# Kernel tuning notes

Measured on AMD Instinct MI355X. Metric: run time of the kernel, lower is better.

Reference implementation:

```python
import jax, jax.numpy as jnp
import numpy as np

N_HEADS, D_MODEL, D_HEAD = 16, 1024, 64
INIT_RANGE = 0.02
BATCH, SEQ = 4, 2048


def setup_inputs() -> dict:
    key = jax.random.key(0)
    k0, k1, k2, k3, k4 = jax.random.split(key, 5)
    resid = jax.random.normal(k0, (BATCH, SEQ, D_MODEL), dtype=jnp.float32)
    w_q = INIT_RANGE * jax.random.normal(k1, (N_HEADS, D_MODEL, D_HEAD), dtype=jnp.float32)
    w_k = INIT_RANGE * jax.random.normal(k2, (N_HEADS, D_MODEL, D_HEAD), dtype=jnp.float32)
    w_v = INIT_RANGE * jax.random.normal(k3, (N_HEADS, D_MODEL, D_HEAD), dtype=jnp.float32)
    w_o = INIT_RANGE * jax.random.normal(k4, (N_HEADS, D_HEAD, D_MODEL), dtype=jnp.float32)
    return {"resid": resid, "w_q": w_q, "w_k": w_k, "w_v": w_v, "w_o": w_o}


def reference(resid, w_q, w_k, w_v, w_o):
    # resid: [b, s, m]; w_q/k/v: [h, m, d]; w_o: [h, d, m]
    qs = jnp.einsum('bsm,hmd->bhsd', resid, w_q)
    ks = jnp.einsum('bsm,hmd->bhsd', resid, w_k)
    vs = jnp.einsum('bsm,hmd->bhsd', resid, w_v)
    attn = jnp.einsum('bhqd,bhkd->bhqk', qs, ks)  # full O(n^2) scores
    s = attn.shape[-1]
    causal = jnp.tril(jnp.ones((s, s), dtype=bool))  # True = keep
    attn = jnp.where(causal, attn, -jnp.inf)
    attn = jax.nn.softmax(attn / jnp.sqrt(jnp.float32(D_HEAD)), axis=-1)
    z = jnp.einsum('bhqk,bhkd->bhqd', attn, vs)
    out = jnp.einsum('bhsd,hdm->bsm', z, w_o)
    return out
```

## Files before the change

kernel.cpp:

```cpp
#include <hip/hip_runtime.h>


typedef __attribute__((ext_vector_type(8))) short short8;
typedef __attribute__((ext_vector_type(4))) float f32x4;
typedef __attribute__((ext_vector_type(16))) float f32x16;

#define GLDS16(g, l) __builtin_amdgcn_global_load_lds(                        \
    (const __attribute__((address_space(1))) unsigned int*)(g),               \
    (__attribute__((address_space(3))) unsigned int*)(l), 16, 0, 0)

static __device__ __forceinline__ unsigned short f2b(float f) {
  union { float f; unsigned u; } c; c.f = f;
  unsigned r = c.u + 0x7fffu + ((c.u >> 16) & 1u);
  return (unsigned short)(r >> 16);
}

static __device__ __forceinline__ int swzc(int row, int c) {
  return (c & ~31) | ((((c >> 3) & 3) ^ ((row >> 1) & 3)) << 3) | (c & 7);
}

__global__ void k_cast(const float* __restrict__ x, unsigned short* __restrict__ o, int n4) {
  int i = blockIdx.x * blockDim.x + threadIdx.x;
  if (i >= n4) return;
  float4 v = reinterpret_cast<const float4*>(x)[i];
  ushort4 u;
  u.x = f2b(v.x); u.y = f2b(v.y); u.z = f2b(v.z); u.w = f2b(v.w);
  const int flat = i * 4;
  const int row = flat >> 10, c = flat & 1023;
  *reinterpret_cast<ushort4*>(&o[row * 1024 + swzc(row, c)]) = u;
}

__global__ void k_trans_qkv(const float* __restrict__ wq, const float* __restrict__ wk,
                            const float* __restrict__ wv, unsigned short* __restrict__ o) {
  __shared__ float t[64][65];
  int blk = blockIdx.x;
  int mt = blk & 15;
  int h = (blk >> 4) & 15;
  int which = blk >> 8;
  const float* w = which == 0 ? wq : (which == 1 ? wk : wv);
  int tid = threadIdx.x;
  int m0 = mt * 64;
  #pragma unroll
  for (int rep = 0; rep < 16; ++rep) {
    int idx = rep * 256 + tid;
    int r = idx >> 6, c = idx & 63;
    t[r][c] = w[(h * 1024 + m0 + r) * 64 + c];
  }
  __syncthreads();
  #pragma unroll
  for (int rep = 0; rep < 16; ++rep) {
    int idx = rep * 256 + tid;
    int dr = idx >> 6, mc = idx & 63;
    const int row = which * 1024 + h * 64 + dr;
    o[row * 1024 + swzc(dr, m0 + mc)] = f2b(t[mc][dr]);
  }
}

__global__ void k_trans_wo(const float* __restrict__ wo, unsigned short* __restrict__ o) {
  __shared__ float t[64][65];
  int blk = blockIdx.x;
  int mt = blk & 15, kt = blk >> 4;
  int tid = threadIdx.x;
  int k0 = kt * 64, m0 = mt * 64;
  #pragma unroll
  for (int rep = 0; rep < 16; ++rep) {
    int idx = rep * 256 + tid;
    int r = idx >> 6, c = idx & 63;
    t[r][c] = wo[(k0 + r) * 1024 + m0 + c];
  }
  __syncthreads();
  #pragma unroll
  for (int rep = 0; rep < 16; ++rep) {
    int idx = rep * 256 + tid;
    int r = idx >> 6, c = idx & 63;
    o[(m0 + r) * 1024 + swzc(r, k0 + c)] = f2b(t[c][r]);
  }
}

__global__ __launch_bounds__(256) void k_gemm_qkv(const unsigned short* __restrict__ A,
                                                  const unsigned short* __restrict__ Bt,
                                                  unsigned short* __restrict__ Qb,
                                                  unsigned short* __restrict__ Kc,
                                                  unsigned short* __restrict__ Vc) {
  __shared__ unsigned short As[2][128 * 32];
  __shared__ unsigned short Bs[2][128 * 32];
  const int bm = blockIdx.x, bn = blockIdx.y;
  const int tid = threadIdx.x;
  const int lane = tid & 63, wid = tid >> 6;
  const int wr = wid >> 1, wc = wid & 1;
  const int fr = lane & 15, fq = lane >> 4;

  f32x4 acc[4][4];
  #pragma unroll
  for (int i = 0; i < 4; ++i)
    #pragma unroll
    for (int n = 0; n < 4; ++n) acc[i][n] = f32x4{0.f, 0.f, 0.f, 0.f};

  const int arow = tid >> 2, acol = (tid & 3) * 8;
  const int lds0 = tid * 8, lds1 = (tid + 256) * 8;
  const unsigned short* aG0 = A + (bm * 128 + arow) * 1024 + acol;
  const unsigned short* aG1 = A + (bm * 128 + arow + 64) * 1024 + acol;
  const unsigned short* bG0 = Bt + (bn * 128 + arow) * 1024 + acol;
  const unsigned short* bG1 = Bt + (bn * 128 + arow + 64) * 1024 + acol;

  const int rowA = (wr * 64 + fr) * 32;
  const int rowB = (wc * 64 + fr) * 32;
  const int slot = ((fq ^ ((fr >> 1) & 3)) << 3);

  for (int k0 = 0; k0 < 1024; k0 += 64) {
    __syncthreads();
    GLDS16(aG0 + k0,      As[0] + lds0);
    GLDS16(aG1 + k0,      As[0] + lds1);
    GLDS16(aG0 + k0 + 32, As[1] + lds0);
    GLDS16(aG1 + k0 + 32, As[1] + lds1);
    GLDS16(bG0 + k0,      Bs[0] + lds0);
    GLDS16(bG1 + k0,      Bs[0] + lds1);
    GLDS16(bG0 + k0 + 32, Bs[1] + lds0);
    GLDS16(bG1 + k0 + 32, Bs[1] + lds1);
    asm volatile("s_waitcnt vmcnt(0)" ::: "memory");
    __syncthreads();
    #pragma unroll
    for (int p = 0; p < 2; ++p) {
      short8 a[4], b[4];
      #pragma unroll
      for (int i = 0; i < 4; ++i)
        a[i] = *reinterpret_cast<const short8*>(As[p] + rowA + i * 512 + slot);
      #pragma unroll
      for (int n = 0; n < 4; ++n)
        b[n] = *reinterpret_cast<const short8*>(Bs[p] + rowB + n * 512 + slot);
      #pragma unroll
      for (int i = 0; i < 4; ++i)
        #pragma unroll
        for (int n = 0; n < 4; ++n)
          acc[i][n] = __builtin_amdgcn_mfma_f32_16x16x32_bf16(a[i], b[n], acc[i][n], 0, 0, 0);
    }
  }

  const float CS = 0.125f * 1.44269504088896340736f;
  const int colb = bn * 128 + wc * 64 + fr;
  const int rowb = bm * 128 + wr * 64 + fq * 4;
  #pragma unroll
  for (int n = 0; n < 4; ++n) {
    const int col = colb + n * 16;
    const int which = col >> 10, rc = col & 1023;
    const int h = rc >> 6, d = rc & 63;
    #pragma unroll
    for (int i = 0; i < 4; ++i) {
      const int row = rowb + i * 16;
      const int b_ = row >> 11, s = row & 2047;
      const int bh = b_ * 16 + h;
      if (which == 2) {
        const int c = s >> 5, kk = s & 31;
        const int r = d >> 1;
        const int sl = (((d & 1) * 4 + (kk >> 3)) ^ (r & 7));
        ushort4 v;
        v.x = f2b(acc[i][n][0]); v.y = f2b(acc[i][n][1]);
        v.z = f2b(acc[i][n][2]); v.w = f2b(acc[i][n][3]);
        *reinterpret_cast<ushort4*>(
            &Vc[((size_t)(bh * 64 + c)) * 2048 + r * 64 + sl * 8 + (kk & 7)]) = v;
      } else if (which == 1) {
        #pragma unroll
        for (int j = 0; j < 4; ++j) {
          const int ss = s + j;
          const int c = ss >> 5, r = ss & 31;
          const int dsw = (((d >> 3) ^ (r & 7)) << 3) | (d & 7);
          Kc[(((size_t)(bh * 64 + c)) * 32 + r) * 64 + dsw] = f2b(acc[i][n][j]);
        }
      } else {
        unsigned short* dst = Qb + ((size_t)bh * 2048 + s) * 64 + d;
        #pragma unroll
        for (int j = 0; j < 4; ++j) dst[j * 64] = f2b(acc[i][n][j] * CS);
      }
    }
  }
}


static __device__ __forceinline__ f32x16 mfma32(short8 a, short8 b, f32x16 c) {
  return __builtin_amdgcn_mfma_f32_32x32x16_bf16(a, b, c, 0, 0, 0);
}

template<bool MASKED>
static __device__ __forceinline__ void compute_chunk(
    const unsigned short* __restrict__ Kl, const unsigned short* __restrict__ Vl,
    int q, int hi,
    const short8& Qf0, const short8& Qf1, const short8& Qf2, const short8& Qf3,
    f32x16& accA, f32x16& accB, float& lsum) {
  const int qs = q & 7;
  const short8 kf0 = *reinterpret_cast<const short8*>(Kl + q * 64 + (((0 + hi) ^ qs) << 3));
  const short8 kf1 = *reinterpret_cast<const short8*>(Kl + q * 64 + (((2 + hi) ^ qs) << 3));
  const short8 kf2 = *reinterpret_cast<const short8*>(Kl + q * 64 + (((4 + hi) ^ qs) << 3));
  const short8 kf3 = *reinterpret_cast<const short8*>(Kl + q * 64 + (((6 + hi) ^ qs) << 3));
  const int vr = q >> 1, vs = (q & 1) * 4, vw = vr & 7;
  const short8 v00 = *reinterpret_cast<const short8*>(Vl + vr * 64 + (((vs + hi) ^ vw) << 3));
  const short8 v01 = *reinterpret_cast<const short8*>(Vl + vr * 64 + (((vs + 2 + hi) ^ vw) << 3));
  const short8 v10 = *reinterpret_cast<const short8*>(Vl + (vr + 16) * 64 + (((vs + hi) ^ vw) << 3));
  const short8 v11 = *reinterpret_cast<const short8*>(Vl + (vr + 16) * 64 + (((vs + 2 + hi) ^ vw) << 3));

  f32x16 s = {0.f,0.f,0.f,0.f,0.f,0.f,0.f,0.f,0.f,0.f,0.f,0.f,0.f,0.f,0.f,0.f};
  s = mfma32(kf0, Qf0, s);
  s = mfma32(kf1, Qf1, s);
  s = mfma32(kf2, Qf2, s);
  s = mfma32(kf3, Qf3, s);

  float p[16];
  #pragma unroll
  for (int r = 0; r < 16; ++r) {
    if (MASKED) {
      const int kr = (r & 3) + 8 * (r >> 2) + 4 * hi;
      p[r] = (kr <= q) ? __builtin_amdgcn_exp2f(s[r]) : 0.f;
    } else {
      p[r] = __builtin_amdgcn_exp2f(s[r]);
    }
  }
  float t0 = (p[0] + p[1]) + (p[2] + p[3]);
  float t1 = (p[4] + p[5]) + (p[6] + p[7]);
  float t2 = (p[8] + p[9]) + (p[10] + p[11]);
  float t3 = (p[12] + p[13]) + (p[14] + p[15]);
  lsum += (t0 + t1) + (t2 + t3);

  unsigned W[8], X[8];
  #pragma unroll
  for (int i = 0; i < 8; ++i)
    asm("v_cvt_pk_bf16_f32 %0, %1, %2" : "=v"(W[i]) : "v"(p[2 * i]), "v"(p[2 * i + 1]));
  #pragma unroll
  for (int i = 0; i < 8; ++i) X[i] = __shfl_xor(W[i], 32);

  union { unsigned u[4]; short8 v; } fa0, fa1;
  fa0.u[0] = hi ? X[2] : W[0];
  fa0.u[1] = hi ? X[3] : W[1];
  fa0.u[2] = hi ? W[2] : X[0];
  fa0.u[3] = hi ? W[3] : X[1];
  fa1.u[0] = hi ? X[6] : W[4];
  fa1.u[1] = hi ? X[7] : W[5];
  fa1.u[2] = hi ? W[6] : X[4];
  fa1.u[3] = hi ? W[7] : X[5];

  accA = mfma32(fa0.v, v00, accA);
  accA = mfma32(fa1.v, v01, accA);
  accB = mfma32(fa0.v, v10, accB);
  accB = mfma32(fa1.v, v11, accB);
}

static __device__ __forceinline__ void store_tile(unsigned short* __restrict__ Zb,
    int b_, int h, int q0, int q, int hi,
    const f32x16& a0, const f32x16& a1, float lsum) {
  const float lt = lsum + __shfl_xor(lsum, 32);
  const float rl = 1.f / lt;
  #pragma unroll
  for (int r = 0; r < 16; ++r) {
    const int qr = (r & 3) + 8 * (r >> 2) + 4 * hi;
    const float rlr = __shfl(rl, qr);
    const int row = b_ * 2048 + q0 + qr;
    const int sl = (((q >> 3) ^ ((qr >> 1) & 3)) << 3) + (q & 7);
    unsigned short* dst = Zb + (size_t)row * 1024 + h * 64;
    dst[sl]      = f2b(a0[r] * rlr);
    dst[32 + sl] = f2b(a1[r] * rlr);
  }
}

__global__ __launch_bounds__(256, 2) void k_attn(const unsigned short* __restrict__ Qb,
                                                 const unsigned short* __restrict__ Kc,
                                                 const unsigned short* __restrict__ Vc,
                                                 unsigned short* __restrict__ Zb) {
  __shared__ __align__(16) unsigned short Kbuf[2][2048];
  __shared__ __align__(16) unsigned short Vbuf[2][2048];
  const int tid = threadIdx.x;
  const int lane = tid & 63, w = tid >> 6;
  const int q = lane & 31, hi = lane >> 5;
  const int bid = blockIdx.x;
  const int bh = (bid & 7) * 8 + ((bid >> 3) & 7);
  const int P1 = bid >> 6;
  const int b_ = bh >> 4, h = bh & 15;

  const unsigned short* Qbh = Qb + (size_t)bh * 2048 * 64;
  const unsigned short* Kch = Kc + (size_t)bh * 64 * 2048;
  const unsigned short* Vch = Vc + (size_t)bh * 64 * 2048;

  #pragma unroll 1
  for (int t = 0; t < 2; ++t) {
    const int P = t ? (15 - P1) : P1;
    const int q0 = 128 * P + 32 * w;
    const int cmax = 4 * P + w;
    const int C = 4 * P + 4;

    const unsigned short* Qp = Qbh + (size_t)(q0 + q) * 64 + hi * 8;
    const short8 Qf0 = *reinterpret_cast<const short8*>(Qp);
    const short8 Qf1 = *reinterpret_cast<const short8*>(Qp + 16);
    const short8 Qf2 = *reinterpret_cast<const short8*>(Qp + 32);
    const short8 Qf3 = *reinterpret_cast<const short8*>(Qp + 48);

    f32x16 a0 = {0.f,0.f,0.f,0.f,0.f,0.f,0.f,0.f,0.f,0.f,0.f,0.f,0.f,0.f,0.f,0.f};
    f32x16 a1 = a0;
    float l = 0.f;

    GLDS16(Kch + tid * 8, &Kbuf[0][tid * 8]);
    GLDS16(Vch + tid * 8, &Vbuf[0][tid * 8]);

    for (int c = 0; c < C; ++c) {
      if (c + 1 < C) {
        const int par = (c + 1) & 1;
        GLDS16(Kch + (size_t)(c + 1) * 2048 + tid * 8, &Kbuf[par][tid * 8]);
        GLDS16(Vch + (size_t)(c + 1) * 2048 + tid * 8, &Vbuf[par][tid * 8]);
        asm volatile("s_waitcnt vmcnt(2)" ::: "memory");
      } else {
        asm volatile("s_waitcnt vmcnt(0)" ::: "memory");
      }
      __syncthreads();
      if (c <= cmax) {
        const int par = c & 1;
        if (c == cmax)
          compute_chunk<true>(Kbuf[par], Vbuf[par], q, hi, Qf0, Qf1, Qf2, Qf3, a0, a1, l);
        else
          compute_chunk<false>(Kbuf[par], Vbuf[par], q, hi, Qf0, Qf1, Qf2, Qf3, a0, a1, l);
      }
      __syncthreads();
    }
    store_tile(Zb, b_, h, q0, q, hi, a0, a1, l);
  }
}

__global__ __launch_bounds__(256) void k_gemm_out(const unsigned short* __restrict__ A,
                                                  const unsigned short* __restrict__ Bt,
                                                  float* __restrict__ Out) {
  __shared__ unsigned short As[2][128 * 32];
  __shared__ unsigned short Bs[2][128 * 32];
  const int bm = blockIdx.x, bn = blockIdx.y;
  const int tid = threadIdx.x;
  const int lane = tid & 63, wid = tid >> 6;
  const int wr = wid >> 1, wc = wid & 1;
  const int fr = lane & 15, fq = lane >> 4;

  f32x4 acc[4][4];
  #pragma unroll
  for (int i = 0; i < 4; ++i)
    #pragma unroll
    for (int n = 0; n < 4; ++n) acc[i][n] = f32x4{0.f, 0.f, 0.f, 0.f};

  const int arow = tid >> 2, acol = (tid & 3) * 8;
  const int lds0 = tid * 8, lds1 = (tid + 256) * 8;
  const unsigned short* aG0 = A + (bm * 128 + arow) * 1024 + acol;
  const unsigned short* aG1 = A + (bm * 128 + arow + 64) * 1024 + acol;
  const unsigned short* bG0 = Bt + (bn * 128 + arow) * 1024 + acol;
  const unsigned short* bG1 = Bt + (bn * 128 + arow + 64) * 1024 + acol;

  const int rowA = (wr * 64 + fr) * 32;
  const int rowB = (wc * 64 + fr) * 32;
  const int slot = ((fq ^ ((fr >> 1) & 3)) << 3);

  for (int k0 = 0; k0 < 1024; k0 += 64) {
    __syncthreads();
    GLDS16(aG0 + k0,      As[0] + lds0);
    GLDS16(aG1 + k0,      As[0] + lds1);
    GLDS16(aG0 + k0 + 32, As[1] + lds0);
    GLDS16(aG1 + k0 + 32, As[1] + lds1);
    GLDS16(bG0 + k0,      Bs[0] + lds0);
    GLDS16(bG1 + k0,      Bs[0] + lds1);
    GLDS16(bG0 + k0 + 32, Bs[1] + lds0);
    GLDS16(bG1 + k0 + 32, Bs[1] + lds1);
    asm volatile("s_waitcnt vmcnt(0)" ::: "memory");
    __syncthreads();
    #pragma unroll
    for (int p = 0; p < 2; ++p) {
      short8 a[4], b[4];
      #pragma unroll
      for (int i = 0; i < 4; ++i)
        a[i] = *reinterpret_cast<const short8*>(As[p] + rowA + i * 512 + slot);
      #pragma unroll
      for (int n = 0; n < 4; ++n)
        b[n] = *reinterpret_cast<const short8*>(Bs[p] + rowB + n * 512 + slot);
      #pragma unroll
      for (int i = 0; i < 4; ++i)
        #pragma unroll
        for (int n = 0; n < 4; ++n)
          acc[i][n] = __builtin_amdgcn_mfma_f32_16x16x32_bf16(a[i], b[n], acc[i][n], 0, 0, 0);
    }
  }

  const int colb = bn * 128 + wc * 64 + fr;
  const int rowb = bm * 128 + wr * 64 + fq * 4;
  #pragma unroll
  for (int n = 0; n < 4; ++n) {
    const int col = colb + n * 16;
    #pragma unroll
    for (int i = 0; i < 4; ++i) {
      const int row = rowb + i * 16;
      #pragma unroll
      for (int j = 0; j < 4; ++j) Out[(size_t)(row + j) * 1024 + col] = acc[i][n][j];
    }
  }
}

extern "C" void kernel_launch(void* const* d_in, const int* in_sizes, int n_in,
                              void* d_out, int out_size, void* d_ws, size_t ws_size,
                              hipStream_t stream) {
  const float* resid = (const float*)d_in[0];
  const float* w_q = (const float*)d_in[1];
  const float* w_k = (const float*)d_in[2];
  const float* w_v = (const float*)d_in[3];
  const float* w_o = (const float*)d_in[4];
  float* out = (float*)d_out;

  char* ws = (char*)d_ws;
  const size_t MB = 1u << 20;
  unsigned short* Xb = (unsigned short*)(ws);
  unsigned short* W3 = (unsigned short*)(ws + 16 * MB);
  unsigned short* Wo = (unsigned short*)(ws + 22 * MB);
  unsigned short* Qb = (unsigned short*)(ws + 24 * MB);
  unsigned short* Kc = (unsigned short*)(ws + 40 * MB);
  unsigned short* Vc = (unsigned short*)(ws + 56 * MB);
  unsigned short* Zb = Xb;

  hipLaunchKernelGGL(k_cast, dim3(8192), dim3(256), 0, stream, resid, Xb, 8192 * 1024 / 4);
  hipLaunchKernelGGL(k_trans_qkv, dim3(768), dim3(256), 0, stream, w_q, w_k, w_v, W3);
  hipLaunchKernelGGL(k_trans_wo, dim3(256), dim3(256), 0, stream, w_o, Wo);
  hipLaunchKernelGGL(k_gemm_qkv, dim3(64, 24), dim3(256), 0, stream, Xb, W3, Qb, Kc, Vc);
  hipLaunchKernelGGL(k_attn, dim3(512), dim3(256), 0, stream, Qb, Kc, Vc, Zb);
  hipLaunchKernelGGL(k_gemm_out, dim3(64, 8), dim3(256), 0, stream, Zb, Wo, out);
}
```

Measured before the change: 168.6 us.

## Double-buffer GEMM K-loop loads and triple-buffer attention K/V chunks

Both GEMM kernels now keep two LDS stage sets, issuing the next 64-wide K slice's global-to-LDS loads before computing on the current one, so memory latency overlaps with MFMA work instead of being waited on serially. The attention kernel moves from double to triple buffering of K/V chunks with a prefetch distance of two, which also drops one barrier per iteration. The cost is more LDS (64KB per GEMM block, 24KB per attention block), which may reduce occupancy.

```diff
diff --git a/kernel.cpp b/kernel.cpp
--- a/kernel.cpp
+++ b/kernel.cpp
@@ -77,13 +77,42 @@
   }
 }
 
+#define QKV_STAGE(k0, SET)                                                    \
+    GLDS16(aG0 + (k0),      As[SET] + lds0);                                  \
+    GLDS16(aG1 + (k0),      As[SET] + lds1);                                  \
+    GLDS16(aG0 + (k0) + 32, As[SET] + 4096 + lds0);                           \
+    GLDS16(aG1 + (k0) + 32, As[SET] + 4096 + lds1);                           \
+    GLDS16(bG0 + (k0),      Bs[SET] + lds0);                                  \
+    GLDS16(bG1 + (k0),      Bs[SET] + lds1);                                  \
+    GLDS16(bG0 + (k0) + 32, Bs[SET] + 4096 + lds0);                           \
+    GLDS16(bG1 + (k0) + 32, Bs[SET] + 4096 + lds1);
+
+#define GEMM_COMPUTE(SET)                                                     \
+    _Pragma("unroll")                                                         \
+    for (int p = 0; p < 2; ++p) {                                             \
+      short8 a[4], b[4];                                                      \
+      _Pragma("unroll")                                                       \
+      for (int i = 0; i < 4; ++i)                                             \
+        a[i] = *reinterpret_cast<const short8*>(As[SET] + p * 4096 + rowA + i * 512 + slot); \
+      _Pragma("unroll")                                                       \
+      for (int n = 0; n < 4; ++n)                                             \
+        b[n] = *reinterpret_cast<const short8*>(Bs[SET] + p * 4096 + rowB + n * 512 + slot); \
+      _Pragma("unroll")                                                       \
+      for (int i = 0; i < 4; ++i)                                             \
+        _Pragma("unroll")                                                     \
+        for (int n = 0; n < 4; ++n)                                           \
+          acc[i][n] = __builtin_amdgcn_mfma_f32_16x16x32_bf16(a[i], b[n], acc[i][n], 0, 0, 0); \
+    }
+
+#define VM0 asm volatile("s_waitcnt vmcnt(0)" ::: "memory")
+
 __global__ __launch_bounds__(256) void k_gemm_qkv(const unsigned short* __restrict__ A,
                                                   const unsigned short* __restrict__ Bt,
                                                   unsigned short* __restrict__ Qb,
                                                   unsigned short* __restrict__ Kc,
                                                   unsigned short* __restrict__ Vc) {
-  __shared__ unsigned short As[2][128 * 32];
-  __shared__ unsigned short Bs[2][128 * 32];
+  __shared__ unsigned short As[2][8192];
+  __shared__ unsigned short Bs[2][8192];
   const int bm = blockIdx.x, bn = blockIdx.y;
   const int tid = threadIdx.x;
   const int lane = tid & 63, wid = tid >> 6;
@@ -107,33 +136,16 @@
   const int rowB = (wc * 64 + fr) * 32;
   const int slot = ((fq ^ ((fr >> 1) & 3)) << 3);
 
-  for (int k0 = 0; k0 < 1024; k0 += 64) {
+  QKV_STAGE(0, 0);
+  for (int s2 = 0; s2 < 16; s2 += 2) {
+    VM0;
     __syncthreads();
-    GLDS16(aG0 + k0,      As[0] + lds0);
-    GLDS16(aG1 + k0,      As[0] + lds1);
-    GLDS16(aG0 + k0 + 32, As[1] + lds0);
-    GLDS16(aG1 + k0 + 32, As[1] + lds1);
-    GLDS16(bG0 + k0,      Bs[0] + lds0);
-    GLDS16(bG1 + k0,      Bs[0] + lds1);
-    GLDS16(bG0 + k0 + 32, Bs[1] + lds0);
-    GLDS16(bG1 + k0 + 32, Bs[1] + lds1);
-    asm volatile("s_waitcnt vmcnt(0)" ::: "memory");
+    QKV_STAGE((s2 + 1) * 64, 1);
+    GEMM_COMPUTE(0);
+    VM0;
     __syncthreads();
-    #pragma unroll
-    for (int p = 0; p < 2; ++p) {
-      short8 a[4], b[4];
-      #pragma unroll
-      for (int i = 0; i < 4; ++i)
-        a[i] = *reinterpret_cast<const short8*>(As[p] + rowA + i * 512 + slot);
-      #pragma unroll
-      for (int n = 0; n < 4; ++n)
-        b[n] = *reinterpret_cast<const short8*>(Bs[p] + rowB + n * 512 + slot);
-      #pragma unroll
-      for (int i = 0; i < 4; ++i)
-        #pragma unroll
-        for (int n = 0; n < 4; ++n)
-          acc[i][n] = __builtin_amdgcn_mfma_f32_16x16x32_bf16(a[i], b[n], acc[i][n], 0, 0, 0);
-    }
+    if (s2 + 2 < 16) { QKV_STAGE((s2 + 2) * 64, 0); }
+    GEMM_COMPUTE(1);
   }
 
   const float CS = 0.125f * 1.44269504088896340736f;
@@ -263,8 +275,8 @@
                                                  const unsigned short* __restrict__ Kc,
                                                  const unsigned short* __restrict__ Vc,
                                                  unsigned short* __restrict__ Zb) {
-  __shared__ __align__(16) unsigned short Kbuf[2][2048];
-  __shared__ __align__(16) unsigned short Vbuf[2][2048];
+  __shared__ __align__(16) unsigned short Kbuf[3][2048];
+  __shared__ __align__(16) unsigned short Vbuf[3][2048];
   const int tid = threadIdx.x;
   const int lane = tid & 63, w = tid >> 6;
   const int q = lane & 31, hi = lane >> 5;
@@ -294,27 +306,29 @@
     f32x16 a1 = a0;
     float l = 0.f;
 
-    GLDS16(Kch + tid * 8, &Kbuf[0][tid * 8]);
-    GLDS16(Vch + tid * 8, &Vbuf[0][tid * 8]);
-
+    __syncthreads();
+    GLDS16(Kch + tid * 8,        &Kbuf[0][tid * 8]);
+    GLDS16(Vch + tid * 8,        &Vbuf[0][tid * 8]);
+    GLDS16(Kch + 2048 + tid * 8, &Kbuf[1][tid * 8]);
+    GLDS16(Vch + 2048 + tid * 8, &Vbuf[1][tid * 8]);
+
+    int ci = 0, si = 2;
     for (int c = 0; c < C; ++c) {
-      if (c + 1 < C) {
-        const int par = (c + 1) & 1;
-        GLDS16(Kch + (size_t)(c + 1) * 2048 + tid * 8, &Kbuf[par][tid * 8]);
-        GLDS16(Vch + (size_t)(c + 1) * 2048 + tid * 8, &Vbuf[par][tid * 8]);
-        asm volatile("s_waitcnt vmcnt(2)" ::: "memory");
-      } else {
-        asm volatile("s_waitcnt vmcnt(0)" ::: "memory");
+      if (c == C - 1) { asm volatile("s_waitcnt vmcnt(0)" ::: "memory"); }
+      else            { asm volatile("s_waitcnt vmcnt(2)" ::: "memory"); }
+      __syncthreads();
+      if (c + 2 < C) {
+        GLDS16(Kch + (size_t)(c + 2) * 2048 + tid * 8, &Kbuf[si][tid * 8]);
+        GLDS16(Vch + (size_t)(c + 2) * 2048 + tid * 8, &Vbuf[si][tid * 8]);
       }
-      __syncthreads();
       if (c <= cmax) {
-        const int par = c & 1;
         if (c == cmax)
-          compute_chunk<true>(Kbuf[par], Vbuf[par], q, hi, Qf0, Qf1, Qf2, Qf3, a0, a1, l);
+          compute_chunk<true>(Kbuf[ci], Vbuf[ci], q, hi, Qf0, Qf1, Qf2, Qf3, a0, a1, l);
         else
-          compute_chunk<false>(Kbuf[par], Vbuf[par], q, hi, Qf0, Qf1, Qf2, Qf3, a0, a1, l);
+          compute_chunk<false>(Kbuf[ci], Vbuf[ci], q, hi, Qf0, Qf1, Qf2, Qf3, a0, a1, l);
       }
-      __syncthreads();
+      ci = (ci + 1 == 3) ? 0 : ci + 1;
+      si = (si + 1 == 3) ? 0 : si + 1;
     }
     store_tile(Zb, b_, h, q0, q, hi, a0, a1, l);
   }
@@ -323,8 +337,8 @@
 __global__ __launch_bounds__(256) void k_gemm_out(const unsigned short* __restrict__ A,
                                                   const unsigned short* __restrict__ Bt,
                                                   float* __restrict__ Out) {
-  __shared__ unsigned short As[2][128 * 32];
-  __shared__ unsigned short Bs[2][128 * 32];
+  __shared__ unsigned short As[2][8192];
+  __shared__ unsigned short Bs[2][8192];
   const int bm = blockIdx.x, bn = blockIdx.y;
   const int tid = threadIdx.x;
   const int lane = tid & 63, wid = tid >> 6;
@@ -348,33 +362,16 @@
   const int rowB = (wc * 64 + fr) * 32;
   const int slot = ((fq ^ ((fr >> 1) & 3)) << 3);
 
-  for (int k0 = 0; k0 < 1024; k0 += 64) {
+  QKV_STAGE(0, 0);
+  for (int s2 = 0; s2 < 16; s2 += 2) {
+    VM0;
     __syncthreads();
-    GLDS16(aG0 + k0,      As[0] + lds0);
-    GLDS16(aG1 + k0,      As[0] + lds1);
-    GLDS16(aG0 + k0 + 32, As[1] + lds0);
-    GLDS16(aG1 + k0 + 32, As[1] + lds1);
-    GLDS16(bG0 + k0,      Bs[0] + lds0);
-    GLDS16(bG1 + k0,      Bs[0] + lds1);
-    GLDS16(bG0 + k0 + 32, Bs[1] + lds0);
-    GLDS16(bG1 + k0 + 32, Bs[1] + lds1);
-    asm volatile("s_waitcnt vmcnt(0)" ::: "memory");
+    QKV_STAGE((s2 + 1) * 64, 1);
+    GEMM_COMPUTE(0);
+    VM0;
     __syncthreads();
-    #pragma unroll
-    for (int p = 0; p < 2; ++p) {
-      short8 a[4], b[4];
-      #pragma unroll
-      for (int i = 0; i < 4; ++i)
-        a[i] = *reinterpret_cast<const short8*>(As[p] + rowA + i * 512 + slot);
-      #pragma unroll
-      for (int n = 0; n < 4; ++n)
-        b[n] = *reinterpret_cast<const short8*>(Bs[p] + rowB + n * 512 + slot);
-      #pragma unroll
-      for (int i = 0; i < 4; ++i)
-        #pragma unroll
-        for (int n = 0; n < 4; ++n)
-          acc[i][n] = __builtin_amdgcn_mfma_f32_16x16x32_bf16(a[i], b[n], acc[i][n], 0, 0, 0);
-    }
+    if (s2 + 2 < 16) { QKV_STAGE((s2 + 2) * 64, 0); }
+    GEMM_COMPUTE(1);
   }
 
   const int colb = bn * 128 + wc * 64 + fr;
```

New measurement: 165.7 us. Within noise of the previous version (-1.7%).

## Fuse paired causal query tiles into one K/V pass with triple-buffered prefetch

Applied to the files above, without the earlier changes.

The attention kernel previously handled its two query tiles (P1 and 15-P1) in sequence, streaming K/V twice. It now keeps both tiles' Q fragments and accumulators live and streams K/V once over the longer tile's range, so each chunk in LDS is shared by both tiles. Staging moves from double to triple buffering with a two-chunk prefetch distance and a single barrier per iteration. The block-to-(bh, P1) mapping is also reordered to interleave light and heavy pairs. The cost is roughly double the accumulator and Q registers per thread, which may put the launch_bounds(256,2) occupancy target or spilling at risk, plus extra LDS.

```diff
diff --git a/kernel.cpp b/kernel.cpp
--- a/kernel.cpp
+++ b/kernel.cpp
@@ -8,6 +8,8 @@
 #define GLDS16(g, l) __builtin_amdgcn_global_load_lds(                        \
     (const __attribute__((address_space(1))) unsigned int*)(g),               \
     (__attribute__((address_space(3))) unsigned int*)(l), 16, 0, 0)
+
+#define VM0 asm volatile("s_waitcnt vmcnt(0)" ::: "memory")
 
 static __device__ __forceinline__ unsigned short f2b(float f) {
   union { float f; unsigned u; } c; c.f = f;
@@ -117,7 +119,7 @@
     GLDS16(bG1 + k0,      Bs[0] + lds1);
     GLDS16(bG0 + k0 + 32, Bs[1] + lds0);
     GLDS16(bG1 + k0 + 32, Bs[1] + lds1);
-    asm volatile("s_waitcnt vmcnt(0)" ::: "memory");
+    VM0;
     __syncthreads();
     #pragma unroll
     for (int p = 0; p < 2; ++p) {
@@ -263,61 +265,76 @@
                                                  const unsigned short* __restrict__ Kc,
                                                  const unsigned short* __restrict__ Vc,
                                                  unsigned short* __restrict__ Zb) {
-  __shared__ __align__(16) unsigned short Kbuf[2][2048];
-  __shared__ __align__(16) unsigned short Vbuf[2][2048];
+  __shared__ __align__(16) unsigned short Kbuf[3][2048];
+  __shared__ __align__(16) unsigned short Vbuf[3][2048];
   const int tid = threadIdx.x;
   const int lane = tid & 63, w = tid >> 6;
   const int q = lane & 31, hi = lane >> 5;
   const int bid = blockIdx.x;
-  const int bh = (bid & 7) * 8 + ((bid >> 3) & 7);
-  const int P1 = bid >> 6;
+  const int g = bid & 7;
+  const int sdec = bid >> 3;
+  const int par = sdec & 1;
+  const int jj = sdec >> 1;
+  const int bh = g * 8 + (jj & 7);
+  const int x = jj >> 3;
+  const int P1 = par ? (7 - x) : x;
+  const int q0A = 128 * P1 + 32 * w;
+  const int q0B = 128 * (15 - P1) + 32 * w;
+  const int cmaxA = 4 * P1 + w;
+  const int cmaxB = 4 * (15 - P1) + w;
+  const int C = 4 * (15 - P1) + 4;
   const int b_ = bh >> 4, h = bh & 15;
 
   const unsigned short* Qbh = Qb + (size_t)bh * 2048 * 64;
   const unsigned short* Kch = Kc + (size_t)bh * 64 * 2048;
   const unsigned short* Vch = Vc + (size_t)bh * 64 * 2048;
 
-  #pragma unroll 1
-  for (int t = 0; t < 2; ++t) {
-    const int P = t ? (15 - P1) : P1;
-    const int q0 = 128 * P + 32 * w;
-    const int cmax = 4 * P + w;
-    const int C = 4 * P + 4;
-
-    const unsigned short* Qp = Qbh + (size_t)(q0 + q) * 64 + hi * 8;
-    const short8 Qf0 = *reinterpret_cast<const short8*>(Qp);
-    const short8 Qf1 = *reinterpret_cast<const short8*>(Qp + 16);
-    const short8 Qf2 = *reinterpret_cast<const short8*>(Qp + 32);
-    const short8 Qf3 = *reinterpret_cast<const short8*>(Qp + 48);
-
-    f32x16 a0 = {0.f,0.f,0.f,0.f,0.f,0.f,0.f,0.f,0.f,0.f,0.f,0.f,0.f,0.f,0.f,0.f};
-    f32x16 a1 = a0;
-    float l = 0.f;
-
-    GLDS16(Kch + tid * 8, &Kbuf[0][tid * 8]);
-    GLDS16(Vch + tid * 8, &Vbuf[0][tid * 8]);
-
-    for (int c = 0; c < C; ++c) {
-      if (c + 1 < C) {
-        const int par = (c + 1) & 1;
-        GLDS16(Kch + (size_t)(c + 1) * 2048 + tid * 8, &Kbuf[par][tid * 8]);
-        GLDS16(Vch + (size_t)(c + 1) * 2048 + tid * 8, &Vbuf[par][tid * 8]);
-        asm volatile("s_waitcnt vmcnt(2)" ::: "memory");
-      } else {
-        asm volatile("s_waitcnt vmcnt(0)" ::: "memory");
-      }
-      __syncthreads();
-      if (c <= cmax) {
-        const int par = c & 1;
-        if (c == cmax)
-          compute_chunk<true>(Kbuf[par], Vbuf[par], q, hi, Qf0, Qf1, Qf2, Qf3, a0, a1, l);
-        else
-          compute_chunk<false>(Kbuf[par], Vbuf[par], q, hi, Qf0, Qf1, Qf2, Qf3, a0, a1, l);
-      }
-      __syncthreads();
-    }
-    store_tile(Zb, b_, h, q0, q, hi, a0, a1, l);
-  }
+  const unsigned short* QpA = Qbh + (size_t)(q0A + q) * 64 + hi * 8;
+  const short8 QA0 = *reinterpret_cast<const short8*>(QpA);
+  const short8 QA1 = *reinterpret_cast<const short8*>(QpA + 16);
+  const short8 QA2 = *reinterpret_cast<const short8*>(QpA + 32);
+  const short8 QA3 = *reinterpret_cast<const short8*>(QpA + 48);
+  const unsigned short* QpB = Qbh + (size_t)(q0B + q) * 64 + hi * 8;
+  const short8 QB0 = *reinterpret_cast<const short8*>(QpB);
+  const short8 QB1 = *reinterpret_cast<const short8*>(QpB + 16);
+  const short8 QB2 = *reinterpret_cast<const short8*>(QpB + 32);
+  const short8 QB3 = *reinterpret_cast<const short8*>(QpB + 48);
+
+  const f32x16 zero = {0.f,0.f,0.f,0.f,0.f,0.f,0.f,0.f,0.f,0.f,0.f,0.f,0.f,0.f,0.f,0.f};
+  f32x16 aA0 = zero, aA1 = zero, aB0 = zero, aB1 = zero;
+  float lA = 0.f, lB = 0.f;
+
+  GLDS16(Kch + tid * 8,        &Kbuf[0][tid * 8]);
+  GLDS16(Vch + tid * 8,        &Vbuf[0][tid * 8]);
+  GLDS16(Kch + 2048 + tid * 8, &Kbuf[1][tid * 8]);
+  GLDS16(Vch + 2048 + tid * 8, &Vbuf[1][tid * 8]);
+
+  int ci = 0, si = 2;
+  for (int c = 0; c < C; ++c) {
+    if (c == C - 1) { VM0; }
+    else            { asm volatile("s_waitcnt vmcnt(2)" ::: "memory"); }
+    __syncthreads();
+    if (c + 2 < C) {
+      GLDS16(Kch + (size_t)(c + 2) * 2048 + tid * 8, &Kbuf[si][tid * 8]);
+      GLDS16(Vch + (size_t)(c + 2) * 2048 + tid * 8, &Vbuf[si][tid * 8]);
+    }
+    if (c <= cmaxA) {
+      if (c == cmaxA)
+        compute_chunk<true >(Kbuf[ci], Vbuf[ci], q, hi, QA0, QA1, QA2, QA3, aA0, aA1, lA);
+      else
+        compute_chunk<false>(Kbuf[ci], Vbuf[ci], q, hi, QA0, QA1, QA2, QA3, aA0, aA1, lA);
+    }
+    if (c <= cmaxB) {
+      if (c == cmaxB)
+        compute_chunk<true >(Kbuf[ci], Vbuf[ci], q, hi, QB0, QB1, QB2, QB3, aB0, aB1, lB);
+      else
+        compute_chunk<false>(Kbuf[ci], Vbuf[ci], q, hi, QB0, QB1, QB2, QB3, aB0, aB1, lB);
+    }
+    ci = (ci + 1 == 3) ? 0 : ci + 1;
+    si = (si + 1 == 3) ? 0 : si + 1;
+  }
+  store_tile(Zb, b_, h, q0A, q, hi, aA0, aA1, lA);
+  store_tile(Zb, b_, h, q0B, q, hi, aB0, aB1, lB);
 }
 
 __global__ __launch_bounds__(256) void k_gemm_out(const unsigned short* __restrict__ A,
@@ -358,7 +375,7 @@
     GLDS16(bG1 + k0,      Bs[0] + lds1);
     GLDS16(bG0 + k0 + 32, Bs[1] + lds0);
     GLDS16(bG1 + k0 + 32, Bs[1] + lds1);
-    asm volatile("s_waitcnt vmcnt(0)" ::: "memory");
+    VM0;
     __syncthreads();
     #pragma unroll
     for (int p = 0; p < 2; ++p) {
```

Measured after the change: 165.0 us. 1.02x faster.
